# Kernel tuning notes

Hardware: AMD Instinct MI355X
Metric: run time of the kernel (lower is better)

The kernel has to match this reference:

```python
import jax, jax.numpy as jnp
import numpy as np

D_PAIR = 128
NUM_HEADS = 4
LN_EPS = 1e-5


def _mha(x, w_in, b_in, w_out, b_out, num_heads):
    # x: [B, R, S, D]; attention over axis S (keys) for each query position.
    B, R, S, D = x.shape
    hd = D // num_heads
    qkv = jnp.einsum('brsd,ed->brse', x, w_in) + b_in  # [B,R,S,3D]
    q, k, v = jnp.split(qkv, 3, axis=-1)
    q = q.reshape(B, R, S, num_heads, hd)
    k = k.reshape(B, R, S, num_heads, hd)
    v = v.reshape(B, R, S, num_heads, hd)
    scores = jnp.einsum('brqhd,brkhd->brhqk', q, k) / jnp.sqrt(jnp.asarray(hd, x.dtype))
    attn = jax.nn.softmax(scores, axis=-1)
    out = jnp.einsum('brhqk,brkhd->brqhd', attn, v).reshape(B, R, S, D)
    return jnp.einsum('brsd,ed->brse', out, w_out) + b_out


def _layernorm(x, gamma, beta):
    mu = jnp.mean(x, axis=-1, keepdims=True)
    var = jnp.mean(jnp.square(x - mu), axis=-1, keepdims=True)
    return (x - mu) * jax.lax.rsqrt(var + LN_EPS) * gamma + beta


def setup_inputs() -> dict:
    key = jax.random.key(0)
    ks = jax.random.split(key, 12)
    B, L, D = 1, 256, D_PAIR
    s = 0.02
    return {
        'pair_repr': jax.random.normal(ks[0], (B, L, L, D), dtype=jnp.float32),
        'chain_id_tensor': jax.random.randint(ks[1], (L,), 0, 2),
        'w_in_s': jax.random.normal(ks[2], (3 * D, D), dtype=jnp.float32) * s,
        'b_in_s': jnp.zeros((3 * D,), jnp.float32),
        'w_out_s': jax.random.normal(ks[3], (D, D), dtype=jnp.float32) * s,
        'b_out_s': jnp.zeros((D,), jnp.float32),
        'w_in_e': jax.random.normal(ks[4], (3 * D, D), dtype=jnp.float32) * s,
        'b_in_e': jnp.zeros((3 * D,), jnp.float32),
        'w_out_e': jax.random.normal(ks[5], (D, D), dtype=jnp.float32) * s,
        'b_out_e': jnp.zeros((D,), jnp.float32),
        'gamma_s': jnp.ones((D,), jnp.float32),
        'beta_s': jnp.zeros((D,), jnp.float32),
        'gamma_e': jnp.ones((D,), jnp.float32),
        'beta_e': jnp.zeros((D,), jnp.float32),
        'w_gate': jax.random.normal(ks[6], (D, D), dtype=jnp.float32) * s,
        'b_gate': jnp.zeros((D,), jnp.float32),
    }


def reference(pair_repr, chain_id_tensor, w_in_s, b_in_s, w_out_s, b_out_s,
              w_in_e, b_in_e, w_out_e, b_out_e, gamma_s, beta_s,
              gamma_e, beta_e, w_gate, b_gate):
    # Row-wise (starting node) attention: attend over axis 2.
    attn_i = _mha(pair_repr, w_in_s, b_in_s, w_out_s, b_out_s, NUM_HEADS)
    pair = _layernorm(pair_repr + attn_i, gamma_s, beta_s)
    # Column-wise (ending node) attention: transpose rows/cols, attend, transpose back.
    pair_t = jnp.swapaxes(pair, 1, 2)
    attn_j = _mha(pair_t, w_in_e, b_in_e, w_out_e, b_out_e, NUM_HEADS)
    pair = _layernorm(pair + jnp.swapaxes(attn_j, 1, 2), gamma_e, beta_e)
    gate = jax.nn.sigmoid(jnp.einsum('bijd,ed->bije', pair, w_gate) + b_gate)
    return pair * gate
```

## Files before the change

### kernel.cpp

```cpp
#include <hip/hip_runtime.h>
#include <hip/hip_bf16.h>
#include <cstddef>

#define DD 128

typedef unsigned short u16;
typedef short short8v __attribute__((ext_vector_type(8)));
typedef float floatx4 __attribute__((ext_vector_type(4)));
typedef float floatx16 __attribute__((ext_vector_type(16)));

__device__ __forceinline__ float bf2f(u16 u) {
    return __uint_as_float(((unsigned int)u) << 16);
}
__device__ __forceinline__ u16 f2b(float x) {
    unsigned u = __float_as_uint(x);
    return (u16)((u + 0x7FFF + ((u >> 16) & 1)) >> 16);
}
__device__ __forceinline__ unsigned cvtpk_bf16(float lo, float hi) {
    unsigned r;
    asm("v_cvt_pk_bf16_f32 %0, %1, %2" : "=v"(r) : "v"(lo), "v"(hi));
    return r;
}

__device__ __forceinline__ void repack16(const floatx16& a, short8v& f0, short8v& f1) {
    unsigned u[8];
    #pragma unroll
    for (int e = 0; e < 4; ++e) {
        u[2*e]   = cvtpk_bf16(a[4*e+0], a[4*e+1]);
        u[2*e+1] = cvtpk_bf16(a[4*e+2], a[4*e+3]);
    }
    #pragma unroll
    for (int be = 0; be < 2; ++be) {
        int a0 = (int)u[4*be+2], b0 = (int)u[4*be+0];
        asm("v_permlane32_swap_b32 %0, %1" : "+v"(a0), "+v"(b0));
        int a1 = (int)u[4*be+3], b1 = (int)u[4*be+1];
        asm("v_permlane32_swap_b32 %0, %1" : "+v"(a1), "+v"(b1));
        union { int i[4]; short8v v; } pu;
        pu.i[0] = b0; pu.i[1] = b1; pu.i[2] = a0; pu.i[3] = a1;
        if (be == 0) f0 = pu.v; else f1 = pu.v;
    }
}

__global__ __launch_bounds__(512) void wcvt_kernel(
    const float* __restrict__ a0, const float* __restrict__ a1,
    const float* __restrict__ a2, const float* __restrict__ a3,
    const float* __restrict__ a4, u16* __restrict__ dst)
{
    int q = blockIdx.x * 512 + threadIdx.x;
    int i = q * 4;
    const float* src; int off;
    if      (i < 49152)  { src = a0; off = 0; }
    else if (i < 65536)  { src = a1; off = 49152; }
    else if (i < 114688) { src = a2; off = 65536; }
    else if (i < 131072) { src = a3; off = 114688; }
    else                 { src = a4; off = 131072; }
    float4 v = *reinterpret_cast<const float4*>(src + (i - off));
    ushort4 o = { f2b(v.x), f2b(v.y), f2b(v.z), f2b(v.w) };
    *reinterpret_cast<ushort4*>(dst + i) = o;
}

__device__ __forceinline__ void stage_wb(const u16* __restrict__ Wb,
                                         u16* __restrict__ Wl, int tid) {
    #pragma unroll
    for (int it = 0; it < 4; ++it) {
        int f = tid + it * 512;
        int row = f >> 4, c8 = f & 15;
        uint4 v = *reinterpret_cast<const uint4*>(Wb + (size_t)row * DD + c8 * 8);
        *reinterpret_cast<uint4*>(&Wl[row * 136 + c8 * 8]) = v;
    }
}

__global__ __launch_bounds__(512, 4) void fused_qkv_attn(
    const float* __restrict__ Xf, const u16* __restrict__ Xb,
    const u16* __restrict__ Wb, const float* __restrict__ bias,
    __hip_bfloat16* __restrict__ O, int swap_store)
{
    constexpr int XP = 136;
    constexpr int KP = 40;
    constexpr int VP = 264;
    __shared__ u16 SMEM[256 * XP];
    u16* X_lds  = SMEM;
    u16* K_lds  = SMEM;
    u16* Vt_lds = SMEM + 256 * KP;

    const int tid = threadIdx.x;
    const int bid = blockIdx.x;
    const int xcd = bid & 7, mm = bid >> 3;
    const int r = xcd * 32 + (mm >> 2);
    const int h = mm & 3;

    if (Xb) {
        const u16* xs = Xb + (size_t)r * 256 * DD;
        #pragma unroll
        for (int it = 0; it < 4; ++it) {
            int f = tid + it * 512, row = f >> 4, c8 = f & 15;
            uint4 v = *reinterpret_cast<const uint4*>(xs + row * DD + c8 * 8);
            *reinterpret_cast<uint4*>(&X_lds[row * XP + c8 * 8]) = v;
        }
    } else {
        const float* xs = Xf + (size_t)r * 256 * DD;
        #pragma unroll
        for (int it = 0; it < 16; ++it) {
            int f = tid + it * 512, row = f >> 5, c4 = f & 31;
            float4 v = *reinterpret_cast<const float4*>(xs + row * DD + c4 * 4);
            ushort4 o = { f2b(v.x), f2b(v.y), f2b(v.z), f2b(v.w) };
            *reinterpret_cast<ushort4*>(&X_lds[row * XP + c4 * 4]) = o;
        }
    }
    __syncthreads();

    const int lane = tid & 63;
    const int wq = tid >> 6;
    const int ql = lane & 31;
    const int hi = lane >> 5;
    const int t0 = wq * 32;

    const u16* Wq = Wb + (size_t)(h * 32) * DD;
    const u16* Wk = Wb + (size_t)(128 + h * 32) * DD;
    const u16* Wv = Wb + (size_t)(256 + h * 32) * DD;

    floatx16 qa, ka, va;
    #pragma unroll
    for (int k2 = 0; k2 < 4; ++k2) {
        int d0 = 8 * k2 + 4 * hi;
        float4 b1 = *reinterpret_cast<const float4*>(bias + h * 32 + d0);
        float4 b2 = *reinterpret_cast<const float4*>(bias + 128 + h * 32 + d0);
        float4 b3 = *reinterpret_cast<const float4*>(bias + 256 + h * 32 + d0);
        qa[4*k2+0] = b1.x; qa[4*k2+1] = b1.y; qa[4*k2+2] = b1.z; qa[4*k2+3] = b1.w;
        ka[4*k2+0] = b2.x; ka[4*k2+1] = b2.y; ka[4*k2+2] = b2.z; ka[4*k2+3] = b2.w;
        va[4*k2+0] = b3.x; va[4*k2+1] = b3.y; va[4*k2+2] = b3.z; va[4*k2+3] = b3.w;
    }

    #pragma unroll
    for (int ks = 0; ks < 8; ++ks) {
        short8v xb = *reinterpret_cast<const short8v*>(
            &X_lds[(t0 + ql) * XP + ks * 16 + hi * 8]);
        short8v aq = *reinterpret_cast<const short8v*>(Wq + (size_t)ql * DD + ks * 16 + hi * 8);
        short8v ak = *reinterpret_cast<const short8v*>(Wk + (size_t)ql * DD + ks * 16 + hi * 8);
        short8v av = *reinterpret_cast<const short8v*>(Wv + (size_t)ql * DD + ks * 16 + hi * 8);
        qa = __builtin_amdgcn_mfma_f32_32x32x16_bf16(aq, xb, qa, 0, 0, 0);
        ka = __builtin_amdgcn_mfma_f32_32x32x16_bf16(ak, xb, ka, 0, 0, 0);
        va = __builtin_amdgcn_mfma_f32_32x32x16_bf16(av, xb, va, 0, 0, 0);
    }

    short8v qf0, qf1, kf0, kf1;
    repack16(qa, qf0, qf1);
    repack16(ka, kf0, kf1);
    u16 vb16[16];
    #pragma unroll
    for (int rr = 0; rr < 16; ++rr) vb16[rr] = f2b(va[rr]);

    __syncthreads();

    *reinterpret_cast<uint4*>(&K_lds[(t0 + ql) * KP + hi * 8]) =
        *reinterpret_cast<const uint4*>(&kf0);
    *reinterpret_cast<uint4*>(&K_lds[(t0 + ql) * KP + 16 + hi * 8]) =
        *reinterpret_cast<const uint4*>(&kf1);
    #pragma unroll
    for (int rr = 0; rr < 16; ++rr)
        Vt_lds[((rr & 3) + 8 * (rr >> 2) + 4 * hi) * VP + t0 + ql] = vb16[rr];
    __syncthreads();

    const float C1 = 0.25505654196988f;
    const floatx16 zf = {0.f,0.f,0.f,0.f,0.f,0.f,0.f,0.f,
                         0.f,0.f,0.f,0.f,0.f,0.f,0.f,0.f};

    floatx16 acc = zf;
    float ell = 0.f;

    __builtin_amdgcn_s_setprio(1);
    #pragma unroll
    for (int b = 0; b < 8; ++b) {
        short8v k0 = *reinterpret_cast<const short8v*>(&K_lds[(32 * b + ql) * KP + hi * 8]);
        short8v k1 = *reinterpret_cast<const short8v*>(&K_lds[(32 * b + ql) * KP + 16 + hi * 8]);
        floatx16 s = zf;
        s = __builtin_amdgcn_mfma_f32_32x32x16_bf16(k0, qf0, s, 0, 0, 0);
        s = __builtin_amdgcn_mfma_f32_32x32x16_bf16(k1, qf1, s, 0, 0, 0);

        unsigned u[8];
        #pragma unroll
        for (int e = 0; e < 4; ++e) {
            float p0 = __builtin_amdgcn_exp2f(s[4*e+0] * C1);
            float p1 = __builtin_amdgcn_exp2f(s[4*e+1] * C1);
            float p2 = __builtin_amdgcn_exp2f(s[4*e+2] * C1);
            float p3 = __builtin_amdgcn_exp2f(s[4*e+3] * C1);
            ell += (p0 + p1) + (p2 + p3);
            u[2*e]     = cvtpk_bf16(p0, p1);
            u[2*e + 1] = cvtpk_bf16(p2, p3);
        }

        #pragma unroll
        for (int be = 0; be < 2; ++be) {
            const int kb = 2 * b + be;
            int a0 = (int)u[4*be + 2], b0 = (int)u[4*be + 0];
            asm("v_permlane32_swap_b32 %0, %1" : "+v"(a0), "+v"(b0));
            int a1 = (int)u[4*be + 3], b1 = (int)u[4*be + 1];
            asm("v_permlane32_swap_b32 %0, %1" : "+v"(a1), "+v"(b1));
            union { int i[4]; short8v v; } pu;
            pu.i[0] = b0; pu.i[1] = b1; pu.i[2] = a0; pu.i[3] = a1;
            short8v vf = *reinterpret_cast<const short8v*>(&Vt_lds[ql * VP + kb * 16 + hi * 8]);
            acc = __builtin_amdgcn_mfma_f32_32x32x16_bf16(vf, pu.v, acc, 0, 0, 0);
        }
    }
    __builtin_amdgcn_s_setprio(0);

    {
        float ex = ell, ey = ell;
        asm("v_permlane32_swap_b32 %0, %1" : "+v"(ex), "+v"(ey));
        ell = ex + ey;
    }

    const float inv = 1.f / ell;
    const int q = t0 + ql;
    const size_t opos = swap_store ? ((size_t)q * 256 + r) : ((size_t)r * 256 + q);
    u16* ob = reinterpret_cast<u16*>(O) + (size_t)h * 2097152 + opos * 32;
    #pragma unroll
    for (int e = 0; e < 4; ++e) {
        ushort4 w = { f2b(acc[4*e+0] * inv), f2b(acc[4*e+1] * inv),
                      f2b(acc[4*e+2] * inv), f2b(acc[4*e+3] * inv) };
        *reinterpret_cast<ushort4*>(ob + e * 8 + hi * 4) = w;
    }
}

__global__ __launch_bounds__(512) void proj_ln_mfma(
    const __hip_bfloat16* __restrict__ A, const u16* __restrict__ Wb,
    const float* __restrict__ bias, const float* __restrict__ RES,
    const float* __restrict__ gamma, const float* __restrict__ beta,
    u16* __restrict__ RESb, u16* __restrict__ Xt)
{
    __shared__ u16 Wl[128 * 136];
    const int tid = threadIdx.x;
    const int tok0 = blockIdx.x * 128;
    const int lane = tid & 63, wq = tid >> 6;
    const int lq = lane & 15, g = lane >> 4;
    const int t = tok0 + wq * 16 + lq;
    const u16* A16 = reinterpret_cast<const u16*>(A);

    stage_wb(Wb, Wl, tid);

    short8v bfrag[4];
    #pragma unroll
    for (int ks = 0; ks < 4; ++ks)
        bfrag[ks] = *reinterpret_cast<const short8v*>(
            A16 + (size_t)ks * 2097152 + (size_t)t * 32 + g * 8);

    __syncthreads();

    floatx4 acc[8];
    #pragma unroll
    for (int et = 0; et < 8; ++et) {
        float4 b4 = *reinterpret_cast<const float4*>(bias + et * 16 + g * 4);
        float4 r4 = *reinterpret_cast<const float4*>(RES + (size_t)t * DD + et * 16 + g * 4);
        acc[et] = { b4.x + r4.x, b4.y + r4.y, b4.z + r4.z, b4.w + r4.w };
        #pragma unroll
        for (int ks = 0; ks < 4; ++ks) {
            short8v afrag = *reinterpret_cast<const short8v*>(
                &Wl[(et * 16 + lq) * 136 + ks * 32 + g * 8]);
            acc[et] = __builtin_amdgcn_mfma_f32_16x16x32_bf16(afrag, bfrag[ks], acc[et], 0, 0, 0);
        }
    }

    float s = 0.f, ss = 0.f;
    #pragma unroll
    for (int et = 0; et < 8; ++et)
        #pragma unroll
        for (int rr = 0; rr < 4; ++rr) { float v = acc[et][rr]; s += v; ss += v * v; }
    s  += __shfl_xor(s, 16);  s  += __shfl_xor(s, 32);
    ss += __shfl_xor(ss, 16); ss += __shfl_xor(ss, 32);
    float mu = s * (1.f / 128.f);
    float var = ss * (1.f / 128.f) - mu * mu;
    float rstd = rsqrtf(var + 1e-5f);

    u16* xt = Xt + (size_t)((t & 255) * 256 + (t >> 8)) * DD;
    u16* rb = RESb + (size_t)t * DD;
    #pragma unroll
    for (int et = 0; et < 8; ++et) {
        float4 g4 = *reinterpret_cast<const float4*>(gamma + et * 16 + g * 4);
        float4 be4 = *reinterpret_cast<const float4*>(beta + et * 16 + g * 4);
        float4 o4;
        o4.x = (acc[et][0] - mu) * rstd * g4.x + be4.x;
        o4.y = (acc[et][1] - mu) * rstd * g4.y + be4.y;
        o4.z = (acc[et][2] - mu) * rstd * g4.z + be4.z;
        o4.w = (acc[et][3] - mu) * rstd * g4.w + be4.w;
        ushort4 xb = { f2b(o4.x), f2b(o4.y), f2b(o4.z), f2b(o4.w) };
        *reinterpret_cast<ushort4*>(&xt[et * 16 + g * 4]) = xb;
        *reinterpret_cast<ushort4*>(&rb[et * 16 + g * 4]) = xb;
    }
}

__global__ __launch_bounds__(512) void proj_ln_gate_mfma(
    const __hip_bfloat16* __restrict__ A, const u16* __restrict__ Wb,
    const float* __restrict__ bias, const u16* __restrict__ RESb,
    const float* __restrict__ gamma, const float* __restrict__ beta,
    const u16* __restrict__ Wgb, const float* __restrict__ bg,
    float* __restrict__ OUT)
{
    __shared__ u16 Wl[128 * 136];
    __shared__ u16 Yl[128 * 136];
    const int tid = threadIdx.x;
    const int tok0 = blockIdx.x * 128;
    const int lane = tid & 63, wq = tid >> 6;
    const int lq = lane & 15, g = lane >> 4;
    const int tl = wq * 16 + lq;
    const int t = tok0 + tl;
    const u16* A16 = reinterpret_cast<const u16*>(A);

    stage_wb(Wb, Wl, tid);

    short8v bfrag[4];
    #pragma unroll
    for (int ks = 0; ks < 4; ++ks)
        bfrag[ks] = *reinterpret_cast<const short8v*>(
            A16 + (size_t)ks * 2097152 + (size_t)t * 32 + g * 8);

    __syncthreads();

    floatx4 acc[8];
    #pragma unroll
    for (int et = 0; et < 8; ++et) {
        float4 b4 = *reinterpret_cast<const float4*>(bias + et * 16 + g * 4);
        ushort4 rv = *reinterpret_cast<const ushort4*>(RESb + (size_t)t * DD + et * 16 + g * 4);
        acc[et] = { b4.x + bf2f(rv.x), b4.y + bf2f(rv.y),
                    b4.z + bf2f(rv.z), b4.w + bf2f(rv.w) };
        #pragma unroll
        for (int ks = 0; ks < 4; ++ks) {
            short8v afrag = *reinterpret_cast<const short8v*>(
                &Wl[(et * 16 + lq) * 136 + ks * 32 + g * 8]);
            acc[et] = __builtin_amdgcn_mfma_f32_16x16x32_bf16(afrag, bfrag[ks], acc[et], 0, 0, 0);
        }
    }

    float s = 0.f, ss = 0.f;
    #pragma unroll
    for (int et = 0; et < 8; ++et)
        #pragma unroll
        for (int rr = 0; rr < 4; ++rr) { float v = acc[et][rr]; s += v; ss += v * v; }
    s  += __shfl_xor(s, 16);  s  += __shfl_xor(s, 32);
    ss += __shfl_xor(ss, 16); ss += __shfl_xor(ss, 32);
    float mu = s * (1.f / 128.f);
    float var = ss * (1.f / 128.f) - mu * mu;
    float rstd = rsqrtf(var + 1e-5f);

    #pragma unroll
    for (int et = 0; et < 8; ++et) {
        float4 g4 = *reinterpret_cast<const float4*>(gamma + et * 16 + g * 4);
        float4 be4 = *reinterpret_cast<const float4*>(beta + et * 16 + g * 4);
        acc[et][0] = (acc[et][0] - mu) * rstd * g4.x + be4.x;
        acc[et][1] = (acc[et][1] - mu) * rstd * g4.y + be4.y;
        acc[et][2] = (acc[et][2] - mu) * rstd * g4.z + be4.z;
        acc[et][3] = (acc[et][3] - mu) * rstd * g4.w + be4.w;
        ushort4 yb;
        yb.x = f2b(acc[et][0]); yb.y = f2b(acc[et][1]);
        yb.z = f2b(acc[et][2]); yb.w = f2b(acc[et][3]);
        *reinterpret_cast<ushort4*>(&Yl[tl * 136 + et * 16 + g * 4]) = yb;
    }

    __syncthreads();
    stage_wb(Wgb, Wl, tid);
    __syncthreads();

    short8v yfrag[4];
    #pragma unroll
    for (int ks = 0; ks < 4; ++ks)
        yfrag[ks] = *reinterpret_cast<const short8v*>(&Yl[tl * 136 + ks * 32 + g * 8]);

    #pragma unroll
    for (int et = 0; et < 8; ++et) {
        float4 b4 = *reinterpret_cast<const float4*>(bg + et * 16 + g * 4);
        floatx4 z = { b4.x, b4.y, b4.z, b4.w };
        #pragma unroll
        for (int ks = 0; ks < 4; ++ks) {
            short8v afrag = *reinterpret_cast<const short8v*>(
                &Wl[(et * 16 + lq) * 136 + ks * 32 + g * 8]);
            z = __builtin_amdgcn_mfma_f32_16x16x32_bf16(afrag, yfrag[ks], z, 0, 0, 0);
        }
        float4 o4;
        o4.x = acc[et][0] / (1.f + __expf(-z[0]));
        o4.y = acc[et][1] / (1.f + __expf(-z[1]));
        o4.z = acc[et][2] / (1.f + __expf(-z[2]));
        o4.w = acc[et][3] / (1.f + __expf(-z[3]));
        *reinterpret_cast<float4*>(OUT + (size_t)t * DD + et * 16 + g * 4) = o4;
    }
}

extern "C" void kernel_launch(void* const* d_in, const int* in_sizes, int n_in,
                              void* d_out, int out_size, void* d_ws, size_t ws_size,
                              hipStream_t stream) {
    const float* pair    = (const float*)d_in[0];
    const float* w_in_s  = (const float*)d_in[2];
    const float* b_in_s  = (const float*)d_in[3];
    const float* w_out_s = (const float*)d_in[4];
    const float* b_out_s = (const float*)d_in[5];
    const float* w_in_e  = (const float*)d_in[6];
    const float* b_in_e  = (const float*)d_in[7];
    const float* w_out_e = (const float*)d_in[8];
    const float* b_out_e = (const float*)d_in[9];
    const float* gamma_s = (const float*)d_in[10];
    const float* beta_s  = (const float*)d_in[11];
    const float* gamma_e = (const float*)d_in[12];
    const float* beta_e  = (const float*)d_in[13];
    const float* w_gate  = (const float*)d_in[14];
    const float* b_gate  = (const float*)d_in[15];
    float* out = (float*)d_out;

    __hip_bfloat16* attn = (__hip_bfloat16*)d_ws;
    u16*            xt   = (u16*)(attn + (size_t)65536 * 128);
    u16*            resb = xt + (size_t)65536 * 128;
    u16*            wb   = resb + (size_t)65536 * 128;

    wcvt_kernel<<<80, 512, 0, stream>>>(w_in_s, w_out_s, w_in_e, w_out_e, w_gate, wb);

    fused_qkv_attn<<<1024, 512, 0, stream>>>(pair, nullptr, wb, b_in_s, attn, 0);
    proj_ln_mfma<<<512, 512, 0, stream>>>(attn, wb + 49152, b_out_s, pair,
                                          gamma_s, beta_s, resb, xt);
    fused_qkv_attn<<<1024, 512, 0, stream>>>(nullptr, xt, wb + 65536, b_in_e, attn, 1);
    proj_ln_gate_mfma<<<512, 512, 0, stream>>>(attn, wb + 114688, b_out_e, resb,
                                               gamma_e, beta_e, wb + 131072, b_gate,
                                               out);
}
```

Before: 126.4 us.

## Pre-convert pair to bf16 and read X directly from global in attention

The fp32 pair tensor is converted to bf16 inside the weight-conversion kernel, which is enlarged to cover it. The attention kernel then loads X fragments straight from global memory instead of staging them through LDS. This removes the X staging buffer and one barrier, so LDS usage drops and the occupancy hint rises from 4 to 6 blocks. The PV accumulation is also split into two independent accumulators to shorten the MFMA dependency chain. In exchange there is an extra full pass that writes bf16 pair to a workspace, and global X loads are strided and repeated across the four head blocks.

```diff
diff --git a/kernel.cpp b/kernel.cpp
--- a/kernel.cpp
+++ b/kernel.cpp
@@ -44,19 +44,29 @@
 __global__ __launch_bounds__(512) void wcvt_kernel(
     const float* __restrict__ a0, const float* __restrict__ a1,
     const float* __restrict__ a2, const float* __restrict__ a3,
-    const float* __restrict__ a4, u16* __restrict__ dst)
+    const float* __restrict__ a4, const float* __restrict__ pair,
+    u16* __restrict__ wdst, u16* __restrict__ pdst)
 {
     int q = blockIdx.x * 512 + threadIdx.x;
-    int i = q * 4;
-    const float* src; int off;
-    if      (i < 49152)  { src = a0; off = 0; }
-    else if (i < 65536)  { src = a1; off = 49152; }
-    else if (i < 114688) { src = a2; off = 65536; }
-    else if (i < 131072) { src = a3; off = 114688; }
-    else                 { src = a4; off = 131072; }
-    float4 v = *reinterpret_cast<const float4*>(src + (i - off));
-    ushort4 o = { f2b(v.x), f2b(v.y), f2b(v.z), f2b(v.w) };
-    *reinterpret_cast<ushort4*>(dst + i) = o;
+    if (q < 40960) {
+        int i = q * 4;
+        const float* src; int off;
+        if      (i < 49152)  { src = a0; off = 0; }
+        else if (i < 65536)  { src = a1; off = 49152; }
+        else if (i < 114688) { src = a2; off = 65536; }
+        else if (i < 131072) { src = a3; off = 114688; }
+        else                 { src = a4; off = 131072; }
+        float4 v = *reinterpret_cast<const float4*>(src + (i - off));
+        ushort4 o = { f2b(v.x), f2b(v.y), f2b(v.z), f2b(v.w) };
+        *reinterpret_cast<ushort4*>(wdst + i) = o;
+    } else {
+        int p = q - 40960;
+        if (p < 2097152) {
+            float4 v = *reinterpret_cast<const float4*>(pair + (size_t)p * 4);
+            ushort4 o = { f2b(v.x), f2b(v.y), f2b(v.z), f2b(v.w) };
+            *reinterpret_cast<ushort4*>(pdst + (size_t)p * 4) = o;
+        }
+    }
 }
 
 __device__ __forceinline__ void stage_wb(const u16* __restrict__ Wb,
@@ -70,18 +80,14 @@
     }
 }
 
-__global__ __launch_bounds__(512, 4) void fused_qkv_attn(
-    const float* __restrict__ Xf, const u16* __restrict__ Xb,
-    const u16* __restrict__ Wb, const float* __restrict__ bias,
-    __hip_bfloat16* __restrict__ O, int swap_store)
+__global__ __launch_bounds__(512, 6) void fused_qkv_attn(
+    const u16* __restrict__ Xb, const u16* __restrict__ Wb,
+    const float* __restrict__ bias, __hip_bfloat16* __restrict__ O, int swap_store)
 {
-    constexpr int XP = 136;
     constexpr int KP = 40;
     constexpr int VP = 264;
-    __shared__ u16 SMEM[256 * XP];
-    u16* X_lds  = SMEM;
-    u16* K_lds  = SMEM;
-    u16* Vt_lds = SMEM + 256 * KP;
+    __shared__ u16 K_lds[256 * KP];
+    __shared__ u16 Vt_lds[32 * VP];
 
     const int tid = threadIdx.x;
     const int bid = blockIdx.x;
@@ -89,32 +95,13 @@
     const int r = xcd * 32 + (mm >> 2);
     const int h = mm & 3;
 
-    if (Xb) {
-        const u16* xs = Xb + (size_t)r * 256 * DD;
-        #pragma unroll
-        for (int it = 0; it < 4; ++it) {
-            int f = tid + it * 512, row = f >> 4, c8 = f & 15;
-            uint4 v = *reinterpret_cast<const uint4*>(xs + row * DD + c8 * 8);
-            *reinterpret_cast<uint4*>(&X_lds[row * XP + c8 * 8]) = v;
-        }
-    } else {
-        const float* xs = Xf + (size_t)r * 256 * DD;
-        #pragma unroll
-        for (int it = 0; it < 16; ++it) {
-            int f = tid + it * 512, row = f >> 5, c4 = f & 31;
-            float4 v = *reinterpret_cast<const float4*>(xs + row * DD + c4 * 4);
-            ushort4 o = { f2b(v.x), f2b(v.y), f2b(v.z), f2b(v.w) };
-            *reinterpret_cast<ushort4*>(&X_lds[row * XP + c4 * 4]) = o;
-        }
-    }
-    __syncthreads();
-
     const int lane = tid & 63;
     const int wq = tid >> 6;
     const int ql = lane & 31;
     const int hi = lane >> 5;
     const int t0 = wq * 32;
 
+    const u16* xs = Xb + (size_t)r * 256 * DD;
     const u16* Wq = Wb + (size_t)(h * 32) * DD;
     const u16* Wk = Wb + (size_t)(128 + h * 32) * DD;
     const u16* Wv = Wb + (size_t)(256 + h * 32) * DD;
@@ -134,7 +121,7 @@
     #pragma unroll
     for (int ks = 0; ks < 8; ++ks) {
         short8v xb = *reinterpret_cast<const short8v*>(
-            &X_lds[(t0 + ql) * XP + ks * 16 + hi * 8]);
+            xs + (size_t)(t0 + ql) * DD + ks * 16 + hi * 8);
         short8v aq = *reinterpret_cast<const short8v*>(Wq + (size_t)ql * DD + ks * 16 + hi * 8);
         short8v ak = *reinterpret_cast<const short8v*>(Wk + (size_t)ql * DD + ks * 16 + hi * 8);
         short8v av = *reinterpret_cast<const short8v*>(Wv + (size_t)ql * DD + ks * 16 + hi * 8);
@@ -146,11 +133,6 @@
     short8v qf0, qf1, kf0, kf1;
     repack16(qa, qf0, qf1);
     repack16(ka, kf0, kf1);
-    u16 vb16[16];
-    #pragma unroll
-    for (int rr = 0; rr < 16; ++rr) vb16[rr] = f2b(va[rr]);
-
-    __syncthreads();
 
     *reinterpret_cast<uint4*>(&K_lds[(t0 + ql) * KP + hi * 8]) =
         *reinterpret_cast<const uint4*>(&kf0);
@@ -158,14 +140,14 @@
         *reinterpret_cast<const uint4*>(&kf1);
     #pragma unroll
     for (int rr = 0; rr < 16; ++rr)
-        Vt_lds[((rr & 3) + 8 * (rr >> 2) + 4 * hi) * VP + t0 + ql] = vb16[rr];
+        Vt_lds[((rr & 3) + 8 * (rr >> 2) + 4 * hi) * VP + t0 + ql] = f2b(va[rr]);
     __syncthreads();
 
     const float C1 = 0.25505654196988f;
     const floatx16 zf = {0.f,0.f,0.f,0.f,0.f,0.f,0.f,0.f,
                          0.f,0.f,0.f,0.f,0.f,0.f,0.f,0.f};
 
-    floatx16 acc = zf;
+    floatx16 acc0 = zf, acc1 = zf;
     float ell = 0.f;
 
     __builtin_amdgcn_s_setprio(1);
@@ -199,7 +181,10 @@
             union { int i[4]; short8v v; } pu;
             pu.i[0] = b0; pu.i[1] = b1; pu.i[2] = a0; pu.i[3] = a1;
             short8v vf = *reinterpret_cast<const short8v*>(&Vt_lds[ql * VP + kb * 16 + hi * 8]);
-            acc = __builtin_amdgcn_mfma_f32_32x32x16_bf16(vf, pu.v, acc, 0, 0, 0);
+            if (be == 0)
+                acc0 = __builtin_amdgcn_mfma_f32_32x32x16_bf16(vf, pu.v, acc0, 0, 0, 0);
+            else
+                acc1 = __builtin_amdgcn_mfma_f32_32x32x16_bf16(vf, pu.v, acc1, 0, 0, 0);
         }
     }
     __builtin_amdgcn_s_setprio(0);
@@ -216,8 +201,10 @@
     u16* ob = reinterpret_cast<u16*>(O) + (size_t)h * 2097152 + opos * 32;
     #pragma unroll
     for (int e = 0; e < 4; ++e) {
-        ushort4 w = { f2b(acc[4*e+0] * inv), f2b(acc[4*e+1] * inv),
-                      f2b(acc[4*e+2] * inv), f2b(acc[4*e+3] * inv) };
+        ushort4 w = { f2b((acc0[4*e+0] + acc1[4*e+0]) * inv),
+                      f2b((acc0[4*e+1] + acc1[4*e+1]) * inv),
+                      f2b((acc0[4*e+2] + acc1[4*e+2]) * inv),
+                      f2b((acc0[4*e+3] + acc1[4*e+3]) * inv) };
         *reinterpret_cast<ushort4*>(ob + e * 8 + hi * 4) = w;
     }
 }
@@ -406,14 +393,16 @@
     __hip_bfloat16* attn = (__hip_bfloat16*)d_ws;
     u16*            xt   = (u16*)(attn + (size_t)65536 * 128);
     u16*            resb = xt + (size_t)65536 * 128;
-    u16*            wb   = resb + (size_t)65536 * 128;
-
-    wcvt_kernel<<<80, 512, 0, stream>>>(w_in_s, w_out_s, w_in_e, w_out_e, w_gate, wb);
-
-    fused_qkv_attn<<<1024, 512, 0, stream>>>(pair, nullptr, wb, b_in_s, attn, 0);
+    u16*            xb0  = resb + (size_t)65536 * 128;
+    u16*            wb   = xb0 + (size_t)65536 * 128;
+
+    wcvt_kernel<<<4176, 512, 0, stream>>>(w_in_s, w_out_s, w_in_e, w_out_e, w_gate,
+                                          pair, wb, xb0);
+
+    fused_qkv_attn<<<1024, 512, 0, stream>>>(xb0, wb, b_in_s, attn, 0);
     proj_ln_mfma<<<512, 512, 0, stream>>>(attn, wb + 49152, b_out_s, pair,
                                           gamma_s, beta_s, resb, xt);
-    fused_qkv_attn<<<1024, 512, 0, stream>>>(nullptr, xt, wb + 65536, b_in_e, attn, 1);
+    fused_qkv_attn<<<1024, 512, 0, stream>>>(xt, wb + 65536, b_in_e, attn, 1);
     proj_ln_gate_mfma<<<512, 512, 0, stream>>>(attn, wb + 114688, b_out_e, resb,
                                                gamma_e, beta_e, wb + 131072, b_gate,
                                                out);
```

New measurement: 137.5 us. +8.9%, slower.
